# Kernel optimization log

Measured on AMD Instinct MI355X. Metric: run time of the kernel, lower is better.

## Reference

```python
import jax, jax.numpy as jnp
import numpy as np

N, E, F_IN, HD, H, G, NG, OUT = 50000, 800000, 128, 64, 4, 512, 50, 64
HC = HD * H  # 256
LN_EPS = 1e-5

def _lin(k, fi, fo):
    return jax.random.normal(k, (fi, fo), jnp.float32) / np.sqrt(fi).astype(np.float32)

def setup_inputs() -> dict:
    key = jax.random.key(0)
    ks = jax.random.split(key, 26)
    x = jax.random.normal(ks[0], (N, F_IN), jnp.float32)
    edge_index = jax.random.randint(ks[1], (2, E), 0, N)
    batch = jnp.sort(jax.random.randint(ks[2], (N,), 0, G))
    group_ids = jax.random.randint(ks[3], (N,), 0, NG)
    inp = {
        'x': x, 'edge_index': edge_index, 'batch': batch, 'group_ids': group_ids,
        'group_table': jax.random.normal(ks[4], (NG, HD), jnp.float32),
        'inW': _lin(ks[5], F_IN + HD, HD), 'inb': jnp.zeros((HD,), jnp.float32),
        'inln_g': jnp.ones((HD,), jnp.float32), 'inln_b': jnp.zeros((HD,), jnp.float32),
        'W0': _lin(ks[6], HD, HC), 'as0': jax.random.normal(ks[7], (H, HD), jnp.float32) * 0.1,
        'ad0': jax.random.normal(ks[8], (H, HD), jnp.float32) * 0.1, 'b0': jnp.zeros((HC,), jnp.float32),
        'ln0g': jnp.ones((HC,), jnp.float32), 'ln0b': jnp.zeros((HC,), jnp.float32),
        'W1': _lin(ks[9], HC, HC), 'as1': jax.random.normal(ks[10], (H, HD), jnp.float32) * 0.1,
        'ad1': jax.random.normal(ks[11], (H, HD), jnp.float32) * 0.1, 'b1': jnp.zeros((HC,), jnp.float32),
        'ln1g': jnp.ones((HC,), jnp.float32), 'ln1b': jnp.zeros((HC,), jnp.float32),
        'fc1W': _lin(ks[12], HC, HD), 'fc1b': jnp.zeros((HD,), jnp.float32),
        'fc2W': _lin(ks[13], HD, OUT), 'fc2b': jnp.zeros((OUT,), jnp.float32),
    }
    return inp

def _layer_norm(x, g, b):
    mu = jnp.mean(x, axis=-1, keepdims=True)
    var = jnp.mean(jnp.square(x - mu), axis=-1, keepdims=True)
    return (x - mu) * jax.lax.rsqrt(var + LN_EPS) * g + b

def _gat_conv(x, src, dst, W, a_src, a_dst, bias):
    # x: [N, Fin] -> per-head projection [N, H, HD]
    xl = (x @ W).reshape(-1, H, HD)
    al_s = jnp.einsum('nhc,hc->nh', xl, a_src)  # [N, H]
    al_d = jnp.einsum('nhc,hc->nh', xl, a_dst)
    e = jax.nn.leaky_relu(al_s[src] + al_d[dst], 0.2)  # [Etot, H]
    m = jax.ops.segment_max(e, dst, num_segments=N)    # stable softmax over in-edges
    ex = jnp.exp(e - m[dst])
    s = jax.ops.segment_sum(ex, dst, num_segments=N)
    alpha = ex / (s[dst] + 1e-16)
    msg = xl[src] * alpha[:, :, None]                   # [Etot, H, HD]
    out = jax.ops.segment_sum(msg, dst, num_segments=N)
    return out.reshape(-1, HC) + bias

def reference(x, edge_index, batch, group_ids, group_table, inW, inb, inln_g, inln_b,
              W0, as0, ad0, b0, ln0g, ln0b, W1, as1, ad1, b1, ln1g, ln1b,
              fc1W, fc1b, fc2W, fc2b):
    # group embedding concat + input projection (Linear -> LN -> GELU)
    h = jnp.concatenate([x, group_table[group_ids]], axis=-1)
    h = jax.nn.gelu(_layer_norm(h @ inW + inb, inln_g, inln_b), approximate=False)
    # add self-loops (PyG GATConv default)
    loop = jnp.arange(N)
    src = jnp.concatenate([edge_index[0], loop])
    dst = jnp.concatenate([edge_index[1], loop])
    # layer 0: dims 64 -> 256, no residual (width mismatch)
    h = jax.nn.gelu(_layer_norm(_gat_conv(h, src, dst, W0, as0, ad0, b0), ln0g, ln0b), approximate=False)
    # layer 1: 256 -> 256, residual applies
    identity = h
    h = jax.nn.gelu(_layer_norm(_gat_conv(h, src, dst, W1, as1, ad1, b1), ln1g, ln1b), approximate=False)
    h = h + identity
    # global mean pool over graphs
    sums = jax.ops.segment_sum(h, batch, num_segments=G)
    cnt = jax.ops.segment_sum(jnp.ones((N, 1), h.dtype), batch, num_segments=G)
    pooled = sums / jnp.maximum(cnt, 1.0)
    z = jax.nn.gelu(pooled @ fc1W + fc1b, approximate=False)
    logits = z @ fc2W + fc2b
    return jax.nn.log_softmax(logits, axis=1)
```

## Files before the change

kernel.cpp:

```cpp
#include <hip/hip_runtime.h>
#include <math.h>

#define N_NODES 50000
#define N_EDGES 800000
#define ETOT (N_EDGES + N_NODES)
#define F_IN 128
#define HD 64
#define NHEAD 4
#define HC 256
#define NGRAPH 512
#define NOUT 64
#define LN_EPS 1e-5f

typedef __attribute__((ext_vector_type(8))) short bf16x8;
typedef __attribute__((ext_vector_type(4))) float f32x4;
typedef __attribute__((ext_vector_type(2))) float f32x2;

__device__ __forceinline__ float wave_sum(float v) {
#pragma unroll
    for (int m = 1; m < 64; m <<= 1) v += __shfl_xor(v, m, 64);
    return v;
}
__device__ __forceinline__ float wave_max(float v) {
#pragma unroll
    for (int m = 1; m < 64; m <<= 1) v = fmaxf(v, __shfl_xor(v, m, 64));
    return v;
}
__device__ __forceinline__ float red16(float v) {
    v += __shfl_xor(v, 1, 64);
    v += __shfl_xor(v, 2, 64);
    v += __shfl_xor(v, 4, 64);
    v += __shfl_xor(v, 8, 64);
    return v;
}
__device__ __forceinline__ float gelu_exact(float x) {
    return 0.5f * x * (1.0f + erff(x * 0.70710678118654752f));
}
__device__ __forceinline__ unsigned short f2bf(float x) {
    unsigned int u = __float_as_uint(x);
    return (unsigned short)((u + 0x7fffu + ((u >> 16) & 1u)) >> 16);
}
__device__ __forceinline__ float bf2f(unsigned short u) {
    return __uint_as_float(((unsigned int)u) << 16);
}

__global__ void k_count(const int* __restrict__ ei, int* __restrict__ deg) {
    int t = blockIdx.x * blockDim.x + threadIdx.x;
    if (t >= ETOT) return;
    int dst = (t < N_EDGES) ? ei[N_EDGES + t] : (t - N_EDGES);
    atomicAdd(deg + dst, 1);
}

__global__ void k_scan(const int* __restrict__ deg, int* __restrict__ rowptr,
                       int* __restrict__ cursor) {
    __shared__ int wsum[16];
    __shared__ int chunk_total;
    int tid = threadIdx.x, wid = tid >> 6, lane = tid & 63;
    int carry = 0;
    if (tid == 0) rowptr[0] = 0;
    for (int base = 0; base < N_NODES; base += 1024) {
        int i = base + tid;
        int v = (i < N_NODES) ? deg[i] : 0;
        int incl = v;
#pragma unroll
        for (int off = 1; off < 64; off <<= 1) {
            int t = __shfl_up(incl, off, 64);
            if (lane >= off) incl += t;
        }
        if (lane == 63) wsum[wid] = incl;
        __syncthreads();
        if (wid == 0) {
            int wv = (lane < 16) ? wsum[lane] : 0;
            int wincl = wv;
#pragma unroll
            for (int off = 1; off < 16; off <<= 1) {
                int t = __shfl_up(wincl, off, 64);
                if (lane >= off) wincl += t;
            }
            if (lane < 16) wsum[lane] = wincl - wv;
            if (lane == 15) chunk_total = wincl;
        }
        __syncthreads();
        int total_incl = carry + wsum[wid] + incl;
        if (i < N_NODES) {
            rowptr[i + 1] = total_incl;
            cursor[i] = total_incl - v;
        }
        carry += chunk_total;
        __syncthreads();
    }
}

__global__ void k_fill(const int* __restrict__ ei, int* __restrict__ cursor,
                       int* __restrict__ csr) {
    int t = blockIdx.x * blockDim.x + threadIdx.x;
    if (t >= ETOT) return;
    int src, dst;
    if (t < N_EDGES) { src = ei[t]; dst = ei[N_EDGES + t]; }
    else             { src = t - N_EDGES; dst = src; }
    int p = atomicAdd(cursor + dst, 1);
    csr[p] = src;
}

__global__ void k_pack_all(const float* __restrict__ inW, const float* __restrict__ W0,
                           const float* __restrict__ W1, const float* __restrict__ as0,
                           const float* __restrict__ ad0,
                           unsigned short* __restrict__ inWpk, unsigned short* __restrict__ W0pk,
                           unsigned short* __restrict__ W1pk, float* __restrict__ us,
                           float* __restrict__ ud) {
    int b = blockIdx.x;
    if (b < 48) {
        int tid = b * 256 + threadIdx.x;
        int i = tid & 7, l = (tid >> 3) & 63, t2 = tid >> 9;
        int nb = t2 % 4, kt = t2 / 4;
        int k = kt * 32 + ((l >> 4) << 3) + i;
        int n = nb * 16 + (l & 15);
        inWpk[tid] = f2bf(inW[k * 64 + n]);
    } else if (b < 112) {
        int tid = (b - 48) * 256 + threadIdx.x;
        int i = tid & 7, l = (tid >> 3) & 63, t2 = tid >> 9;
        int nb = t2 % 16, kt = t2 / 16;
        int q = kt * 32 + ((l >> 4) << 3) + i;
        int k = 16 * (q & 3) + (q >> 2);
        int n = nb * 16 + (l & 15);
        W0pk[tid] = f2bf(W0[k * 256 + n]);
    } else if (b < 368) {
        int tid = (b - 112) * 256 + threadIdx.x;
        int i = tid & 7, l = (tid >> 3) & 63, t2 = tid >> 9;
        int nb = t2 % 16, kt = t2 / 16;
        int k = kt * 32 + ((l >> 4) << 3) + i;
        int n = nb * 16 + (l & 15);
        W1pk[tid] = f2bf(W1[k * 256 + n]);
    } else {
        int t = threadIdx.x;
        int h = t >> 6, k2 = t & 63;
        float ss = 0.f, dd = 0.f;
        for (int c = 0; c < 64; c++) {
            float w = W0[k2 * 256 + h * 64 + c];
            ss += w * as0[h * 64 + c];
            dd += w * ad0[h * 64 + c];
        }
        us[t] = ss;
        ud[t] = dd;
    }
}

__global__ void k_proj_in_mma(const float* __restrict__ x, const int* __restrict__ gid,
                              const float* __restrict__ gt,
                              const unsigned short* __restrict__ Wpk,
                              const float* __restrict__ inb, const float* __restrict__ lng,
                              const float* __restrict__ lnb, const float* __restrict__ us,
                              const float* __restrict__ ud, unsigned int* __restrict__ h08,
                              float* __restrict__ als0, float* __restrict__ ald0) {
    int wid = threadIdx.x >> 6, lane = threadIdx.x & 63;
    int m0 = blockIdx.x * 64 + wid * 16;
    if (m0 >= N_NODES) return;
    int g16 = lane >> 4, c16 = lane & 15;
    int row_a = m0 + c16;
    int g = gid[row_a];
    f32x4 acc[4] = {{0,0,0,0},{0,0,0,0},{0,0,0,0},{0,0,0,0}};
#pragma unroll
    for (int kt = 0; kt < 6; kt++) {
        const float* src = (kt < 4) ? (x + (size_t)row_a * F_IN + kt * 32 + g16 * 8)
                                    : (gt + (size_t)g * HD + (kt - 4) * 32 + g16 * 8);
        float4 f0 = *(const float4*)(src);
        float4 f1 = *(const float4*)(src + 4);
        bf16x8 a;
        a[0] = (short)f2bf(f0.x); a[1] = (short)f2bf(f0.y);
        a[2] = (short)f2bf(f0.z); a[3] = (short)f2bf(f0.w);
        a[4] = (short)f2bf(f1.x); a[5] = (short)f2bf(f1.y);
        a[6] = (short)f2bf(f1.z); a[7] = (short)f2bf(f1.w);
#pragma unroll
        for (int nt = 0; nt < 4; nt++) {
            bf16x8 b = *(const bf16x8*)(Wpk + (((kt * 4 + nt) * 64 + lane) << 3));
            acc[nt] = __builtin_amdgcn_mfma_f32_16x16x32_bf16(a, b, acc[nt], 0, 0, 0);
        }
    }
    float bv[4], gv[4], bb[4];
    float usl[4][4], udl[4][4];
#pragma unroll
    for (int nt = 0; nt < 4; nt++) {
        int c = nt * 16 + c16;
        bv[nt] = inb[c]; gv[nt] = lng[c]; bb[nt] = lnb[c];
#pragma unroll
        for (int h = 0; h < 4; h++) {
            usl[h][nt] = us[h * 64 + c];
            udl[h][nt] = ud[h * 64 + c];
        }
    }
#pragma unroll
    for (int j = 0; j < 4; j++) {
        float d[4], s = 0.f;
#pragma unroll
        for (int nt = 0; nt < 4; nt++) { d[nt] = acc[nt][j] + bv[nt]; s += d[nt]; }
        float mu = red16(s) * (1.0f / 64.0f);
        float v = 0.f;
#pragma unroll
        for (int nt = 0; nt < 4; nt++) { d[nt] -= mu; v += d[nt] * d[nt]; }
        float r = rsqrtf(red16(v) * (1.0f / 64.0f) + LN_EPS);
        int row = m0 + g16 * 4 + j;
        float y0 = gelu_exact(d[0] * r * gv[0] + bb[0]);
        float y1 = gelu_exact(d[1] * r * gv[1] + bb[1]);
        float y2 = gelu_exact(d[2] * r * gv[2] + bb[2]);
        float y3 = gelu_exact(d[3] * r * gv[3] + bb[3]);
        int u = __builtin_amdgcn_cvt_pk_fp8_f32(y0, y1, 0, false);
        u = __builtin_amdgcn_cvt_pk_fp8_f32(y2, y3, u, true);
        h08[(size_t)row * 16 + c16] = (unsigned int)u;
        float ps0 = y0 * usl[0][0] + y1 * usl[0][1] + y2 * usl[0][2] + y3 * usl[0][3];
        float ps1 = y0 * usl[1][0] + y1 * usl[1][1] + y2 * usl[1][2] + y3 * usl[1][3];
        float ps2 = y0 * usl[2][0] + y1 * usl[2][1] + y2 * usl[2][2] + y3 * usl[2][3];
        float ps3 = y0 * usl[3][0] + y1 * usl[3][1] + y2 * usl[3][2] + y3 * usl[3][3];
        float pd0 = y0 * udl[0][0] + y1 * udl[0][1] + y2 * udl[0][2] + y3 * udl[0][3];
        float pd1 = y0 * udl[1][0] + y1 * udl[1][1] + y2 * udl[1][2] + y3 * udl[1][3];
        float pd2 = y0 * udl[2][0] + y1 * udl[2][1] + y2 * udl[2][2] + y3 * udl[2][3];
        float pd3 = y0 * udl[3][0] + y1 * udl[3][1] + y2 * udl[3][2] + y3 * udl[3][3];
        ps0 = red16(ps0); ps1 = red16(ps1); ps2 = red16(ps2); ps3 = red16(ps3);
        pd0 = red16(pd0); pd1 = red16(pd1); pd2 = red16(pd2); pd3 = red16(pd3);
        if (c16 == 0) {
            float4 s4 = {ps0, ps1, ps2, ps3};
            float4 d4 = {pd0, pd1, pd2, pd3};
            ((float4*)als0)[row] = s4;
            ((float4*)ald0)[row] = d4;
        }
    }
}

__global__ void k_agg0(const int* __restrict__ rowptr, const int* __restrict__ csr,
                       const unsigned int* __restrict__ h08, const float* __restrict__ als,
                       const float* __restrict__ ald, unsigned short* __restrict__ aggbf) {
    __shared__ float4 lacc[2][64];
    __shared__ float lss[2][4];
    int wid = threadIdx.x >> 6, lane = threadIdx.x & 63;
    int nloc = wid >> 1, half = wid & 1;
    int node = blockIdx.x * 2 + nloc;
    int start = rowptr[node], end = rowptr[node + 1];
    int g = lane >> 4, l16 = lane & 15;
    float4 adv = ((const float4*)ald)[node];
    int cntE = end - start;
    int mid = start + ((cntE + 1) >> 1);
    int k0 = half ? mid : start;
    int k1 = half ? end : mid;
    float a00 = 0, a01 = 0, a02 = 0, a03 = 0;
    float a10 = 0, a11 = 0, a12 = 0, a13 = 0;
    float a20 = 0, a21 = 0, a22 = 0, a23 = 0;
    float a30 = 0, a31 = 0, a32 = 0, a33 = 0;
    float s0 = 0, s1 = 0, s2 = 0, s3 = 0;
    const float4* als4 = (const float4*)als;
    for (int kb = k0; kb < k1; kb += 8) {
        int eA = kb + g, eB = kb + 4 + g;
        int cA = (eA < k1) ? eA : (k1 - 1);
        int cB = (eB < k1) ? eB : (k1 - 1);
        int snA = csr[cA], snB = csr[cB];
        float4 avA = als4[snA], avB = als4[snB];
        unsigned int uA = h08[(size_t)snA * 16 + l16];
        unsigned int uB = h08[(size_t)snB * 16 + l16];
        float eA0 = avA.x + adv.x; eA0 = fmaxf(eA0, 0.2f * eA0);
        float eA1 = avA.y + adv.y; eA1 = fmaxf(eA1, 0.2f * eA1);
        float eA2 = avA.z + adv.z; eA2 = fmaxf(eA2, 0.2f * eA2);
        float eA3 = avA.w + adv.w; eA3 = fmaxf(eA3, 0.2f * eA3);
        float wA0 = __expf(eA0), wA1 = __expf(eA1), wA2 = __expf(eA2), wA3 = __expf(eA3);
        if (eA >= k1) { wA0 = 0.f; wA1 = 0.f; wA2 = 0.f; wA3 = 0.f; }
        f32x2 loA = __builtin_amdgcn_cvt_pk_f32_fp8((int)uA, false);
        f32x2 hiA = __builtin_amdgcn_cvt_pk_f32_fp8((int)uA, true);
        s0 += wA0; s1 += wA1; s2 += wA2; s3 += wA3;
        float x0 = loA.x, x1 = loA.y, x2 = hiA.x, x3 = hiA.y;
        a00 += wA0 * x0; a01 += wA0 * x1; a02 += wA0 * x2; a03 += wA0 * x3;
        a10 += wA1 * x0; a11 += wA1 * x1; a12 += wA1 * x2; a13 += wA1 * x3;
        a20 += wA2 * x0; a21 += wA2 * x1; a22 += wA2 * x2; a23 += wA2 * x3;
        a30 += wA3 * x0; a31 += wA3 * x1; a32 += wA3 * x2; a33 += wA3 * x3;
        float eB0 = avB.x + adv.x; eB0 = fmaxf(eB0, 0.2f * eB0);
        float eB1 = avB.y + adv.y; eB1 = fmaxf(eB1, 0.2f * eB1);
        float eB2 = avB.z + adv.z; eB2 = fmaxf(eB2, 0.2f * eB2);
        float eB3 = avB.w + adv.w; eB3 = fmaxf(eB3, 0.2f * eB3);
        float wB0 = __expf(eB0), wB1 = __expf(eB1), wB2 = __expf(eB2), wB3 = __expf(eB3);
        if (eB >= k1) { wB0 = 0.f; wB1 = 0.f; wB2 = 0.f; wB3 = 0.f; }
        f32x2 loB = __builtin_amdgcn_cvt_pk_f32_fp8((int)uB, false);
        f32x2 hiB = __builtin_amdgcn_cvt_pk_f32_fp8((int)uB, true);
        s0 += wB0; s1 += wB1; s2 += wB2; s3 += wB3;
        float z0 = loB.x, z1 = loB.y, z2 = hiB.x, z3 = hiB.y;
        a00 += wB0 * z0; a01 += wB0 * z1; a02 += wB0 * z2; a03 += wB0 * z3;
        a10 += wB1 * z0; a11 += wB1 * z1; a12 += wB1 * z2; a13 += wB1 * z3;
        a20 += wB2 * z0; a21 += wB2 * z1; a22 += wB2 * z2; a23 += wB2 * z3;
        a30 += wB3 * z0; a31 += wB3 * z1; a32 += wB3 * z2; a33 += wB3 * z3;
    }
#define RED2(v) v += __shfl_xor(v, 16, 64); v += __shfl_xor(v, 32, 64)
    RED2(a00); RED2(a01); RED2(a02); RED2(a03);
    RED2(a10); RED2(a11); RED2(a12); RED2(a13);
    RED2(a20); RED2(a21); RED2(a22); RED2(a23);
    RED2(a30); RED2(a31); RED2(a32); RED2(a33);
    RED2(s0);  RED2(s1);  RED2(s2);  RED2(s3);
#undef RED2
    if (half) {
        float o0 = (g == 0) ? a00 : (g == 1) ? a10 : (g == 2) ? a20 : a30;
        float o1 = (g == 0) ? a01 : (g == 1) ? a11 : (g == 2) ? a21 : a31;
        float o2 = (g == 0) ? a02 : (g == 1) ? a12 : (g == 2) ? a22 : a32;
        float o3 = (g == 0) ? a03 : (g == 1) ? a13 : (g == 2) ? a23 : a33;
        float4 o = {o0, o1, o2, o3};
        lacc[nloc][lane] = o;
        if (lane < 4) {
            float sv = (lane == 0) ? s0 : (lane == 1) ? s1 : (lane == 2) ? s2 : s3;
            lss[nloc][lane] = sv;
        }
    }
    __syncthreads();
    if (!half) {
        float4 p0 = lacc[nloc][0 + l16];
        float4 p1 = lacc[nloc][16 + l16];
        float4 p2 = lacc[nloc][32 + l16];
        float4 p3 = lacc[nloc][48 + l16];
        a00 += p0.x; a01 += p0.y; a02 += p0.z; a03 += p0.w;
        a10 += p1.x; a11 += p1.y; a12 += p1.z; a13 += p1.w;
        a20 += p2.x; a21 += p2.y; a22 += p2.z; a23 += p2.w;
        a30 += p3.x; a31 += p3.y; a32 += p3.z; a33 += p3.w;
        s0 += lss[nloc][0]; s1 += lss[nloc][1];
        s2 += lss[nloc][2]; s3 += lss[nloc][3];
        float o0 = (g == 0) ? a00 : (g == 1) ? a10 : (g == 2) ? a20 : a30;
        float o1 = (g == 0) ? a01 : (g == 1) ? a11 : (g == 2) ? a21 : a31;
        float o2 = (g == 0) ? a02 : (g == 1) ? a12 : (g == 2) ? a22 : a32;
        float o3 = (g == 0) ? a03 : (g == 1) ? a13 : (g == 2) ? a23 : a33;
        float sg = (g == 0) ? s0 : (g == 1) ? s1 : (g == 2) ? s2 : s3;
        float inv = 1.0f / (sg + 1e-16f);
        ushort4 o = {f2bf(o0 * inv), f2bf(o1 * inv), f2bf(o2 * inv), f2bf(o3 * inv)};
        ((ushort4*)aggbf)[(size_t)node * 64 + lane] = o;
    }
}

__global__ void k_postgemm0(const unsigned short* __restrict__ A,
                            const unsigned short* __restrict__ Wpk,
                            const float* __restrict__ bias, const float* __restrict__ lng,
                            const float* __restrict__ lnb, unsigned short* __restrict__ h1bf) {
    int wid = threadIdx.x >> 6, lane = threadIdx.x & 63;
    int m0 = blockIdx.x * 64 + wid * 16;
    if (m0 >= N_NODES) return;
    int g16 = lane >> 4, c16 = lane & 15;
    f32x4 acc[16] = {};
#pragma unroll
    for (int h = 0; h < 4; h++) {
#pragma unroll
        for (int kt = 0; kt < 2; kt++) {
            bf16x8 a = *(const bf16x8*)(A + (size_t)(m0 + c16) * 256 + h * 64 + kt * 32 + g16 * 8);
#pragma unroll
            for (int nt = 0; nt < 4; nt++) {
                bf16x8 b = *(const bf16x8*)(Wpk + (((kt * 16 + h * 4 + nt) * 64 + lane) << 3));
                acc[h * 4 + nt] = __builtin_amdgcn_mfma_f32_16x16x32_bf16(a, b, acc[h * 4 + nt], 0, 0, 0);
            }
        }
    }
    float bv[16], gv[16], bb[16];
#pragma unroll
    for (int q = 0; q < 16; q++) {
        int c = q * 16 + c16;
        bv[q] = bias[c]; gv[q] = lng[c]; bb[q] = lnb[c];
    }
#pragma unroll
    for (int j = 0; j < 4; j++) {
        float d[16], ssum = 0.f;
#pragma unroll
        for (int q = 0; q < 16; q++) { d[q] = acc[q][j] + bv[q]; ssum += d[q]; }
        float mu = red16(ssum) * (1.0f / 256.0f);
        float v = 0.f;
#pragma unroll
        for (int q = 0; q < 16; q++) { d[q] -= mu; v += d[q] * d[q]; }
        float r = rsqrtf(red16(v) * (1.0f / 256.0f) + LN_EPS);
        int row = m0 + g16 * 4 + j;
#pragma unroll
        for (int q = 0; q < 16; q++) {
            float y = gelu_exact(d[q] * r * gv[q] + bb[q]);
            h1bf[(size_t)row * 256 + q * 16 + c16] = f2bf(y);
        }
    }
}

__global__ void k_proj_mma(const unsigned short* __restrict__ A,
                           const unsigned short* __restrict__ Wpk,
                           const float* __restrict__ as_, const float* __restrict__ ad_,
                           unsigned int* __restrict__ xl8, float* __restrict__ als,
                           float* __restrict__ ald) {
    int wid = threadIdx.x >> 6, lane = threadIdx.x & 63;
    int m0 = blockIdx.x * 16;
    int g16 = lane >> 4, c16 = lane & 15;
    f32x4 acc[4] = {{0,0,0,0},{0,0,0,0},{0,0,0,0},{0,0,0,0}};
#pragma unroll
    for (int kt = 0; kt < 8; kt++) {
        bf16x8 a = *(const bf16x8*)(A + (size_t)(m0 + c16) * 256 + kt * 32 + g16 * 8);
#pragma unroll
        for (int nt = 0; nt < 4; nt++) {
            bf16x8 b = *(const bf16x8*)(Wpk + (((kt * 16 + wid * 4 + nt) * 64 + lane) << 3));
            acc[nt] = __builtin_amdgcn_mfma_f32_16x16x32_bf16(a, b, acc[nt], 0, 0, 0);
        }
    }
    float asv[4], adv[4];
#pragma unroll
    for (int nt = 0; nt < 4; nt++) {
        int c = wid * 64 + nt * 16 + c16;
        asv[nt] = as_[c]; adv[nt] = ad_[c];
    }
#pragma unroll
    for (int j = 0; j < 4; j++) {
        int row = m0 + g16 * 4 + j;
        float v0 = acc[0][j], v1 = acc[1][j], v2 = acc[2][j], v3 = acc[3][j];
        int u = __builtin_amdgcn_cvt_pk_fp8_f32(v0, v1, 0, false);
        u = __builtin_amdgcn_cvt_pk_fp8_f32(v2, v3, u, true);
        xl8[(size_t)row * 64 + wid * 16 + c16] = (unsigned int)u;
        float ps = v0 * asv[0] + v1 * asv[1] + v2 * asv[2] + v3 * asv[3];
        float pd = v0 * adv[0] + v1 * adv[1] + v2 * adv[2] + v3 * adv[3];
        ps = red16(ps); pd = red16(pd);
        if (c16 == 0) { als[row * 4 + wid] = ps; ald[row * 4 + wid] = pd; }
    }
}

__global__ void k_agg1(const int* __restrict__ rowptr, const int* __restrict__ csr,
                       const unsigned int* __restrict__ xl8, const float* __restrict__ als,
                       const float* __restrict__ ald, const float* __restrict__ bias,
                       const float* __restrict__ lng, const float* __restrict__ lnb,
                       const unsigned short* __restrict__ identity_bf,
                       const int* __restrict__ batch, float* __restrict__ pooled,
                       int* __restrict__ cnt) {
    __shared__ float4 lacc[2][3][64];
    __shared__ float lss[2][3][64];
    __shared__ float4 lyout[2][64];
    __shared__ int lbatch[2];
    int wid = threadIdx.x >> 6, lane = threadIdx.x & 63;
    int nloc = wid >> 2, q = wid & 3;
    int node = blockIdx.x * 2 + nloc;
    int start = rowptr[node], end = rowptr[node + 1];
    int len = end - start;
    int head = lane >> 4, c16 = lane & 15;
    int fb = head * 64 + c16;
    float adh = ald[node * 4 + head];
    int k0 = start + (len * q) / 4;
    int k1 = start + (len * (q + 1)) / 4;
    float4 acc = {0.f, 0.f, 0.f, 0.f};
    float s = 0.f;
    int k = k0;
    for (; k + 4 <= k1; k += 4) {
        int sn0 = csr[k], sn1 = csr[k + 1], sn2 = csr[k + 2], sn3 = csr[k + 3];
        float e0 = als[sn0 * 4 + head] + adh;
        float e1 = als[sn1 * 4 + head] + adh;
        float e2 = als[sn2 * 4 + head] + adh;
        float e3 = als[sn3 * 4 + head] + adh;
        unsigned int u0 = xl8[(size_t)sn0 * 64 + lane];
        unsigned int u1 = xl8[(size_t)sn1 * 64 + lane];
        unsigned int u2 = xl8[(size_t)sn2 * 64 + lane];
        unsigned int u3 = xl8[(size_t)sn3 * 64 + lane];
        e0 = fmaxf(e0, 0.2f * e0); e1 = fmaxf(e1, 0.2f * e1);
        e2 = fmaxf(e2, 0.2f * e2); e3 = fmaxf(e3, 0.2f * e3);
        float a0 = __expf(e0), a1 = __expf(e1), a2 = __expf(e2), a3 = __expf(e3);
        s += a0 + a1 + a2 + a3;
        f32x2 lo0 = __builtin_amdgcn_cvt_pk_f32_fp8((int)u0, false);
        f32x2 hi0 = __builtin_amdgcn_cvt_pk_f32_fp8((int)u0, true);
        f32x2 lo1 = __builtin_amdgcn_cvt_pk_f32_fp8((int)u1, false);
        f32x2 hi1 = __builtin_amdgcn_cvt_pk_f32_fp8((int)u1, true);
        f32x2 lo2 = __builtin_amdgcn_cvt_pk_f32_fp8((int)u2, false);
        f32x2 hi2 = __builtin_amdgcn_cvt_pk_f32_fp8((int)u2, true);
        f32x2 lo3 = __builtin_amdgcn_cvt_pk_f32_fp8((int)u3, false);
        f32x2 hi3 = __builtin_amdgcn_cvt_pk_f32_fp8((int)u3, true);
        acc.x += a0 * lo0.x + a1 * lo1.x + a2 * lo2.x + a3 * lo3.x;
        acc.y += a0 * lo0.y + a1 * lo1.y + a2 * lo2.y + a3 * lo3.y;
        acc.z += a0 * hi0.x + a1 * hi1.x + a2 * hi2.x + a3 * hi3.x;
        acc.w += a0 * hi0.y + a1 * hi1.y + a2 * hi2.y + a3 * hi3.y;
    }
    for (; k < k1; k++) {
        int sn = csr[k];
        float e = als[sn * 4 + head] + adh;
        e = fmaxf(e, 0.2f * e);
        float a = __expf(e);
        s += a;
        unsigned int u = xl8[(size_t)sn * 64 + lane];
        f32x2 lo = __builtin_amdgcn_cvt_pk_f32_fp8((int)u, false);
        f32x2 hi = __builtin_amdgcn_cvt_pk_f32_fp8((int)u, true);
        acc.x += a * lo.x; acc.y += a * lo.y;
        acc.z += a * hi.x; acc.w += a * hi.y;
    }
    if (q) { lacc[nloc][q - 1][lane] = acc; lss[nloc][q - 1][lane] = s; }
    __syncthreads();
    if (q == 0) {
        float4 p0 = lacc[nloc][0][lane];
        float4 p1 = lacc[nloc][1][lane];
        float4 p2 = lacc[nloc][2][lane];
        acc.x += p0.x + p1.x + p2.x;
        acc.y += p0.y + p1.y + p2.y;
        acc.z += p0.z + p1.z + p2.z;
        acc.w += p0.w + p1.w + p2.w;
        s += lss[nloc][0][lane] + lss[nloc][1][lane] + lss[nloc][2][lane];
        float inv = 1.0f / (s + 1e-16f);
        acc.x = acc.x * inv + bias[fb];
        acc.y = acc.y * inv + bias[fb + 16];
        acc.z = acc.z * inv + bias[fb + 32];
        acc.w = acc.w * inv + bias[fb + 48];
        float mu = wave_sum(acc.x + acc.y + acc.z + acc.w) * (1.0f / 256.0f);
        float dx = acc.x - mu, dy = acc.y - mu, dz = acc.z - mu, dw = acc.w - mu;
        float var = wave_sum(dx * dx + dy * dy + dz * dz + dw * dw) * (1.0f / 256.0f);
        float r = rsqrtf(var + LN_EPS);
        float g0v = lng[fb], g1v = lng[fb + 16], g2v = lng[fb + 32], g3v = lng[fb + 48];
        float b0v = lnb[fb], b1v = lnb[fb + 16], b2v = lnb[fb + 32], b3v = lnb[fb + 48];
        const unsigned short* idp = identity_bf + (size_t)node * 256 + fb;
        float4 y;
        y.x = gelu_exact(dx * r * g0v + b0v) + bf2f(idp[0]);
        y.y = gelu_exact(dy * r * g1v + b1v) + bf2f(idp[16]);
        y.z = gelu_exact(dz * r * g2v + b2v) + bf2f(idp[32]);
        y.w = gelu_exact(dw * r * g3v + b3v) + bf2f(idp[48]);
        lyout[nloc][lane] = y;
        if (lane == 0) lbatch[nloc] = batch[node];
    }
    __syncthreads();
    if (wid == 0) {
        int g0 = lbatch[0], g1 = lbatch[1];
        float4 a = lyout[0][lane], b = lyout[1][lane];
        float* p0 = pooled + (size_t)g0 * 256 + fb;
        if (g0 == g1) {
            atomicAdd(p0 +  0, a.x + b.x); atomicAdd(p0 + 16, a.y + b.y);
            atomicAdd(p0 + 32, a.z + b.z); atomicAdd(p0 + 48, a.w + b.w);
            if (lane == 0) atomicAdd(cnt + g0, 2);
        } else {
            float* p1 = pooled + (size_t)g1 * 256 + fb;
            atomicAdd(p0 +  0, a.x); atomicAdd(p0 + 16, a.y);
            atomicAdd(p0 + 32, a.z); atomicAdd(p0 + 48, a.w);
            atomicAdd(p1 +  0, b.x); atomicAdd(p1 + 16, b.y);
            atomicAdd(p1 + 32, b.z); atomicAdd(p1 + 48, b.w);
            if (lane == 0) { atomicAdd(cnt + g0, 1); atomicAdd(cnt + g1, 1); }
        }
    }
}

__global__ void k_final(const float* __restrict__ pooled, const int* __restrict__ cnt,
                        const float* __restrict__ fc1W, const float* __restrict__ fc1b,
                        const float* __restrict__ fc2W, const float* __restrict__ fc2b,
                        float* __restrict__ out) {
    __shared__ float prow[4][256];
    __shared__ float zrow[4][64];
    int wid = threadIdx.x >> 6, lane = threadIdx.x & 63;
    int g = blockIdx.x * 4 + wid;
    float inv = 1.0f / fmaxf((float)cnt[g], 1.0f);
#pragma unroll
    for (int k = lane; k < 256; k += 64) prow[wid][k] = pooled[g * 256 + k] * inv;
    __syncthreads();
    float acc = fc1b[lane];
#pragma unroll 4
    for (int k = 0; k < 256; k++) acc += prow[wid][k] * fc1W[k * 64 + lane];
    zrow[wid][lane] = gelu_exact(acc);
    __syncthreads();
    float logit = fc2b[lane];
#pragma unroll 4
    for (int k = 0; k < 64; k++) logit += zrow[wid][k] * fc2W[k * 64 + lane];
    float mx = wave_max(logit);
    float se = wave_sum(__expf(logit - mx));
    out[g * NOUT + lane] = logit - mx - logf(se);
}

extern "C" void kernel_launch(void* const* d_in, const int* in_sizes, int n_in,
                              void* d_out, int out_size, void* d_ws, size_t ws_size,
                              hipStream_t stream) {
    const float* x     = (const float*)d_in[0];
    const int*   ei    = (const int*)d_in[1];
    const int*   batch = (const int*)d_in[2];
    const int*   gid   = (const int*)d_in[3];
    const float* gt    = (const float*)d_in[4];
    const float* inW   = (const float*)d_in[5];
    const float* inb   = (const float*)d_in[6];
    const float* inlng = (const float*)d_in[7];
    const float* inlnb = (const float*)d_in[8];
    const float* W0    = (const float*)d_in[9];
    const float* as0   = (const float*)d_in[10];
    const float* ad0   = (const float*)d_in[11];
    const float* b0    = (const float*)d_in[12];
    const float* ln0g  = (const float*)d_in[13];
    const float* ln0b  = (const float*)d_in[14];
    const float* W1    = (const float*)d_in[15];
    const float* as1   = (const float*)d_in[16];
    const float* ad1   = (const float*)d_in[17];
    const float* b1    = (const float*)d_in[18];
    const float* ln1g  = (const float*)d_in[19];
    const float* ln1b  = (const float*)d_in[20];
    const float* fc1W  = (const float*)d_in[21];
    const float* fc1b  = (const float*)d_in[22];
    const float* fc2W  = (const float*)d_in[23];
    const float* fc2b  = (const float*)d_in[24];
    float* out = (float*)d_out;

    char* ws = (char*)d_ws;
    size_t off = 0;
    auto alloc = [&](size_t bytes) {
        void* p = ws + off;
        off += (bytes + 255) / 256 * 256;
        return p;
    };
    unsigned int*   h08    = (unsigned int*)alloc((size_t)N_NODES * 16 * 4);
    unsigned short* agg0bf = (unsigned short*)alloc((size_t)N_NODES * 256 * 2);
    unsigned short* h1bf   = (unsigned short*)alloc((size_t)N_NODES * 256 * 2);
    unsigned int*   xl8    = (unsigned int*)alloc((size_t)N_NODES * 64 * 4);
    unsigned short* inWpk  = (unsigned short*)alloc((size_t)192 * 64 * 2);
    unsigned short* W0pk   = (unsigned short*)alloc((size_t)64 * 256 * 2);
    unsigned short* W1pk   = (unsigned short*)alloc((size_t)256 * 256 * 2);
    float* us     = (float*)alloc((size_t)256 * 4);
    float* ud     = (float*)alloc((size_t)256 * 4);
    float* als0   = (float*)alloc((size_t)N_NODES * 4 * 4);
    float* ald0   = (float*)alloc((size_t)N_NODES * 4 * 4);
    float* als1   = (float*)alloc((size_t)N_NODES * 4 * 4);
    float* ald1   = (float*)alloc((size_t)N_NODES * 4 * 4);
    int*   rowptr = (int*)alloc((size_t)(N_NODES + 1) * 4);
    int*   cursor = (int*)alloc((size_t)N_NODES * 4);
    int*   csr    = (int*)alloc((size_t)ETOT * 4);
    float* pooled = (float*)alloc((size_t)NGRAPH * 256 * 4);
    int*   cnt    = (int*)alloc((size_t)NGRAPH * 4);
    int*   deg    = (int*)alloc((size_t)N_NODES * 4);
    size_t zspan = ((char*)deg + (size_t)N_NODES * 4) - (char*)pooled;

    hipMemsetAsync(pooled, 0, zspan, stream);

    int eb = (ETOT + 255) / 256;
    k_count<<<eb, 256, 0, stream>>>(ei, deg);
    k_scan<<<1, 1024, 0, stream>>>(deg, rowptr, cursor);
    k_fill<<<eb, 256, 0, stream>>>(ei, cursor, csr);

    k_pack_all<<<369, 256, 0, stream>>>(inW, W0, W1, as0, ad0, inWpk, W0pk, W1pk, us, ud);

    k_proj_in_mma<<<(N_NODES + 63) / 64, 256, 0, stream>>>(x, gid, gt, inWpk, inb, inlng, inlnb,
                                                           us, ud, h08, als0, ald0);
    k_agg0<<<N_NODES / 2, 256, 0, stream>>>(rowptr, csr, h08, als0, ald0, agg0bf);
    k_postgemm0<<<(N_NODES + 63) / 64, 256, 0, stream>>>(agg0bf, W0pk, b0, ln0g, ln0b, h1bf);
    k_proj_mma<<<N_NODES / 16, 256, 0, stream>>>(h1bf, W1pk, as1, ad1, xl8, als1, ald1);
    k_agg1<<<N_NODES / 2, 512, 0, stream>>>(rowptr, csr, xl8, als1, ald1, b1, ln1g, ln1b,
                                            h1bf, batch, pooled, cnt);
    k_final<<<NGRAPH / 4, 256, 0, stream>>>(pooled, cnt, fc1W, fc1b, fc2W, fc2b, out);
}
```

Before: 435.6 us.

## Split layer-1 aggregation into per-head gather kernel and separate LN/pool kernel

Replaces the fused layer-1 aggregation with two kernels. The first gives each head its own block, splits edges between two waves, and has each 16-lane group take one edge so four edges are gathered at once. It writes normalized per-head sums as bf16 to a new buffer. The second kernel applies bias, LayerNorm, GELU and the residual, then pools with atomics, merging four nodes into one atomic when they share a graph. This aims to raise gather parallelism and cut per-block reduction overhead, at the cost of an extra global round trip and a kernel launch.

```diff
diff --git a/kernel.cpp b/kernel.cpp
--- a/kernel.cpp
+++ b/kernel.cpp
@@ -409,117 +409,120 @@
     }
 }
 
-__global__ void k_agg1(const int* __restrict__ rowptr, const int* __restrict__ csr,
-                       const unsigned int* __restrict__ xl8, const float* __restrict__ als,
-                       const float* __restrict__ ald, const float* __restrict__ bias,
-                       const float* __restrict__ lng, const float* __restrict__ lnb,
-                       const unsigned short* __restrict__ identity_bf,
-                       const int* __restrict__ batch, float* __restrict__ pooled,
-                       int* __restrict__ cnt) {
-    __shared__ float4 lacc[2][3][64];
-    __shared__ float lss[2][3][64];
-    __shared__ float4 lyout[2][64];
-    __shared__ int lbatch[2];
+__global__ void k_agg1g(const int* __restrict__ rowptr, const int* __restrict__ csr,
+                        const unsigned int* __restrict__ xl8, const float* __restrict__ als,
+                        const float* __restrict__ ald, unsigned short* __restrict__ partial) {
+    __shared__ float4 lacc[2][16];
+    __shared__ float lssm[2][16];
+    int bid = blockIdx.x;
+    int h = bid & 3;
+    int pair = bid >> 2;
     int wid = threadIdx.x >> 6, lane = threadIdx.x & 63;
-    int nloc = wid >> 2, q = wid & 3;
-    int node = blockIdx.x * 2 + nloc;
+    int nloc = wid >> 1, half = wid & 1;
+    int node = pair * 2 + nloc;
     int start = rowptr[node], end = rowptr[node + 1];
-    int len = end - start;
+    int g = lane >> 4, l16 = lane & 15;
+    float adh = ald[node * 4 + h];
+    int cntE = end - start;
+    int mid = start + ((cntE + 1) >> 1);
+    int k0 = half ? mid : start;
+    int k1 = half ? end : mid;
+    float a0 = 0, a1 = 0, a2 = 0, a3 = 0, s = 0;
+    for (int kb = k0; kb < k1; kb += 8) {
+        int eA = kb + g, eB = kb + 4 + g;
+        int cA = (eA < k1) ? eA : (k1 - 1);
+        int cB = (eB < k1) ? eB : (k1 - 1);
+        int snA = csr[cA], snB = csr[cB];
+        float evA = als[snA * 4 + h] + adh;
+        float evB = als[snB * 4 + h] + adh;
+        unsigned int uA = xl8[(size_t)snA * 64 + h * 16 + l16];
+        unsigned int uB = xl8[(size_t)snB * 64 + h * 16 + l16];
+        evA = fmaxf(evA, 0.2f * evA);
+        evB = fmaxf(evB, 0.2f * evB);
+        float wA = __expf(evA), wB = __expf(evB);
+        if (eA >= k1) wA = 0.f;
+        if (eB >= k1) wB = 0.f;
+        f32x2 loA = __builtin_amdgcn_cvt_pk_f32_fp8((int)uA, false);
+        f32x2 hiA = __builtin_amdgcn_cvt_pk_f32_fp8((int)uA, true);
+        f32x2 loB = __builtin_amdgcn_cvt_pk_f32_fp8((int)uB, false);
+        f32x2 hiB = __builtin_amdgcn_cvt_pk_f32_fp8((int)uB, true);
+        s += wA + wB;
+        a0 += wA * loA.x + wB * loB.x;
+        a1 += wA * loA.y + wB * loB.y;
+        a2 += wA * hiA.x + wB * hiB.x;
+        a3 += wA * hiA.y + wB * hiB.y;
+    }
+    a0 += __shfl_xor(a0, 16, 64); a0 += __shfl_xor(a0, 32, 64);
+    a1 += __shfl_xor(a1, 16, 64); a1 += __shfl_xor(a1, 32, 64);
+    a2 += __shfl_xor(a2, 16, 64); a2 += __shfl_xor(a2, 32, 64);
+    a3 += __shfl_xor(a3, 16, 64); a3 += __shfl_xor(a3, 32, 64);
+    s  += __shfl_xor(s, 16, 64);  s  += __shfl_xor(s, 32, 64);
+    if (half && g == 0) {
+        float4 o = {a0, a1, a2, a3};
+        lacc[nloc][l16] = o;
+        lssm[nloc][l16] = s;
+    }
+    __syncthreads();
+    if (!half && g == 0) {
+        float4 p = lacc[nloc][l16];
+        a0 += p.x; a1 += p.y; a2 += p.z; a3 += p.w;
+        s += lssm[nloc][l16];
+        float inv = 1.0f / (s + 1e-16f);
+        ushort4 o = {f2bf(a0 * inv), f2bf(a1 * inv), f2bf(a2 * inv), f2bf(a3 * inv)};
+        ((ushort4*)partial)[(size_t)node * 64 + h * 16 + l16] = o;
+    }
+}
+
+__global__ void k_ln1(const unsigned short* __restrict__ partial, const float* __restrict__ bias,
+                      const float* __restrict__ lng, const float* __restrict__ lnb,
+                      const unsigned short* __restrict__ identity_bf,
+                      const int* __restrict__ batch, float* __restrict__ pooled,
+                      int* __restrict__ cnt) {
+    __shared__ float4 ly[4][64];
+    __shared__ int lb[4];
+    int wid = threadIdx.x >> 6, lane = threadIdx.x & 63;
+    int node = blockIdx.x * 4 + wid;
     int head = lane >> 4, c16 = lane & 15;
     int fb = head * 64 + c16;
-    float adh = ald[node * 4 + head];
-    int k0 = start + (len * q) / 4;
-    int k1 = start + (len * (q + 1)) / 4;
-    float4 acc = {0.f, 0.f, 0.f, 0.f};
-    float s = 0.f;
-    int k = k0;
-    for (; k + 4 <= k1; k += 4) {
-        int sn0 = csr[k], sn1 = csr[k + 1], sn2 = csr[k + 2], sn3 = csr[k + 3];
-        float e0 = als[sn0 * 4 + head] + adh;
-        float e1 = als[sn1 * 4 + head] + adh;
-        float e2 = als[sn2 * 4 + head] + adh;
-        float e3 = als[sn3 * 4 + head] + adh;
-        unsigned int u0 = xl8[(size_t)sn0 * 64 + lane];
-        unsigned int u1 = xl8[(size_t)sn1 * 64 + lane];
-        unsigned int u2 = xl8[(size_t)sn2 * 64 + lane];
-        unsigned int u3 = xl8[(size_t)sn3 * 64 + lane];
-        e0 = fmaxf(e0, 0.2f * e0); e1 = fmaxf(e1, 0.2f * e1);
-        e2 = fmaxf(e2, 0.2f * e2); e3 = fmaxf(e3, 0.2f * e3);
-        float a0 = __expf(e0), a1 = __expf(e1), a2 = __expf(e2), a3 = __expf(e3);
-        s += a0 + a1 + a2 + a3;
-        f32x2 lo0 = __builtin_amdgcn_cvt_pk_f32_fp8((int)u0, false);
-        f32x2 hi0 = __builtin_amdgcn_cvt_pk_f32_fp8((int)u0, true);
-        f32x2 lo1 = __builtin_amdgcn_cvt_pk_f32_fp8((int)u1, false);
-        f32x2 hi1 = __builtin_amdgcn_cvt_pk_f32_fp8((int)u1, true);
-        f32x2 lo2 = __builtin_amdgcn_cvt_pk_f32_fp8((int)u2, false);
-        f32x2 hi2 = __builtin_amdgcn_cvt_pk_f32_fp8((int)u2, true);
-        f32x2 lo3 = __builtin_amdgcn_cvt_pk_f32_fp8((int)u3, false);
-        f32x2 hi3 = __builtin_amdgcn_cvt_pk_f32_fp8((int)u3, true);
-        acc.x += a0 * lo0.x + a1 * lo1.x + a2 * lo2.x + a3 * lo3.x;
-        acc.y += a0 * lo0.y + a1 * lo1.y + a2 * lo2.y + a3 * lo3.y;
-        acc.z += a0 * hi0.x + a1 * hi1.x + a2 * hi2.x + a3 * hi3.x;
-        acc.w += a0 * hi0.y + a1 * hi1.y + a2 * hi2.y + a3 * hi3.y;
-    }
-    for (; k < k1; k++) {
-        int sn = csr[k];
-        float e = als[sn * 4 + head] + adh;
-        e = fmaxf(e, 0.2f * e);
-        float a = __expf(e);
-        s += a;
-        unsigned int u = xl8[(size_t)sn * 64 + lane];
-        f32x2 lo = __builtin_amdgcn_cvt_pk_f32_fp8((int)u, false);
-        f32x2 hi = __builtin_amdgcn_cvt_pk_f32_fp8((int)u, true);
-        acc.x += a * lo.x; acc.y += a * lo.y;
-        acc.z += a * hi.x; acc.w += a * hi.y;
-    }
-    if (q) { lacc[nloc][q - 1][lane] = acc; lss[nloc][q - 1][lane] = s; }
+    ushort4 pv = ((const ushort4*)partial)[(size_t)node * 64 + lane];
+    float ax = bf2f(pv.x) + bias[fb];
+    float ay = bf2f(pv.y) + bias[fb + 16];
+    float az = bf2f(pv.z) + bias[fb + 32];
+    float aw = bf2f(pv.w) + bias[fb + 48];
+    float mu = wave_sum(ax + ay + az + aw) * (1.0f / 256.0f);
+    float dx = ax - mu, dy = ay - mu, dz = az - mu, dw = aw - mu;
+    float var = wave_sum(dx * dx + dy * dy + dz * dz + dw * dw) * (1.0f / 256.0f);
+    float r = rsqrtf(var + LN_EPS);
+    float g0v = lng[fb], g1v = lng[fb + 16], g2v = lng[fb + 32], g3v = lng[fb + 48];
+    float b0v = lnb[fb], b1v = lnb[fb + 16], b2v = lnb[fb + 32], b3v = lnb[fb + 48];
+    const unsigned short* idp = identity_bf + (size_t)node * 256 + fb;
+    float4 y;
+    y.x = gelu_exact(dx * r * g0v + b0v) + bf2f(idp[0]);
+    y.y = gelu_exact(dy * r * g1v + b1v) + bf2f(idp[16]);
+    y.z = gelu_exact(dz * r * g2v + b2v) + bf2f(idp[32]);
+    y.w = gelu_exact(dw * r * g3v + b3v) + bf2f(idp[48]);
+    int b = batch[node];
+    ly[wid][lane] = y;
+    if (lane == 0) lb[wid] = b;
     __syncthreads();
-    if (q == 0) {
-        float4 p0 = lacc[nloc][0][lane];
-        float4 p1 = lacc[nloc][1][lane];
-        float4 p2 = lacc[nloc][2][lane];
-        acc.x += p0.x + p1.x + p2.x;
-        acc.y += p0.y + p1.y + p2.y;
-        acc.z += p0.z + p1.z + p2.z;
-        acc.w += p0.w + p1.w + p2.w;
-        s += lss[nloc][0][lane] + lss[nloc][1][lane] + lss[nloc][2][lane];
-        float inv = 1.0f / (s + 1e-16f);
-        acc.x = acc.x * inv + bias[fb];
-        acc.y = acc.y * inv + bias[fb + 16];
-        acc.z = acc.z * inv + bias[fb + 32];
-        acc.w = acc.w * inv + bias[fb + 48];
-        float mu = wave_sum(acc.x + acc.y + acc.z + acc.w) * (1.0f / 256.0f);
-        float dx = acc.x - mu, dy = acc.y - mu, dz = acc.z - mu, dw = acc.w - mu;
-        float var = wave_sum(dx * dx + dy * dy + dz * dz + dw * dw) * (1.0f / 256.0f);
-        float r = rsqrtf(var + LN_EPS);
-        float g0v = lng[fb], g1v = lng[fb + 16], g2v = lng[fb + 32], g3v = lng[fb + 48];
-        float b0v = lnb[fb], b1v = lnb[fb + 16], b2v = lnb[fb + 32], b3v = lnb[fb + 48];
-        const unsigned short* idp = identity_bf + (size_t)node * 256 + fb;
-        float4 y;
-        y.x = gelu_exact(dx * r * g0v + b0v) + bf2f(idp[0]);
-        y.y = gelu_exact(dy * r * g1v + b1v) + bf2f(idp[16]);
-        y.z = gelu_exact(dz * r * g2v + b2v) + bf2f(idp[32]);
-        y.w = gelu_exact(dw * r * g3v + b3v) + bf2f(idp[48]);
-        lyout[nloc][lane] = y;
-        if (lane == 0) lbatch[nloc] = batch[node];
-    }
-    __syncthreads();
-    if (wid == 0) {
-        int g0 = lbatch[0], g1 = lbatch[1];
-        float4 a = lyout[0][lane], b = lyout[1][lane];
-        float* p0 = pooled + (size_t)g0 * 256 + fb;
-        if (g0 == g1) {
-            atomicAdd(p0 +  0, a.x + b.x); atomicAdd(p0 + 16, a.y + b.y);
-            atomicAdd(p0 + 32, a.z + b.z); atomicAdd(p0 + 48, a.w + b.w);
-            if (lane == 0) atomicAdd(cnt + g0, 2);
-        } else {
-            float* p1 = pooled + (size_t)g1 * 256 + fb;
-            atomicAdd(p0 +  0, a.x); atomicAdd(p0 + 16, a.y);
-            atomicAdd(p0 + 32, a.z); atomicAdd(p0 + 48, a.w);
-            atomicAdd(p1 +  0, b.x); atomicAdd(p1 + 16, b.y);
-            atomicAdd(p1 + 32, b.z); atomicAdd(p1 + 48, b.w);
-            if (lane == 0) { atomicAdd(cnt + g0, 1); atomicAdd(cnt + g1, 1); }
-        }
+    bool merged = (lb[0] == lb[1]) && (lb[1] == lb[2]) && (lb[2] == lb[3]);
+    if (merged) {
+        if (wid == 0) {
+            float4 y0 = ly[0][lane], y1 = ly[1][lane], y2 = ly[2][lane], y3 = ly[3][lane];
+            float* p = pooled + (size_t)lb[0] * 256 + fb;
+            atomicAdd(p +  0, y0.x + y1.x + y2.x + y3.x);
+            atomicAdd(p + 16, y0.y + y1.y + y2.y + y3.y);
+            atomicAdd(p + 32, y0.z + y1.z + y2.z + y3.z);
+            atomicAdd(p + 48, y0.w + y1.w + y2.w + y3.w);
+            if (lane == 0) atomicAdd(cnt + lb[0], 4);
+        }
+    } else {
+        float* p = pooled + (size_t)b * 256 + fb;
+        atomicAdd(p +  0, y.x);
+        atomicAdd(p + 16, y.y);
+        atomicAdd(p + 32, y.z);
+        atomicAdd(p + 48, y.w);
+        if (lane == 0) atomicAdd(cnt + b, 1);
     }
 }
 
@@ -589,6 +592,7 @@
     unsigned short* agg0bf = (unsigned short*)alloc((size_t)N_NODES * 256 * 2);
     unsigned short* h1bf   = (unsigned short*)alloc((size_t)N_NODES * 256 * 2);
     unsigned int*   xl8    = (unsigned int*)alloc((size_t)N_NODES * 64 * 4);
+    unsigned short* part1  = (unsigned short*)alloc((size_t)N_NODES * 256 * 2);
     unsigned short* inWpk  = (unsigned short*)alloc((size_t)192 * 64 * 2);
     unsigned short* W0pk   = (unsigned short*)alloc((size_t)64 * 256 * 2);
     unsigned short* W1pk   = (unsigned short*)alloc((size_t)256 * 256 * 2);
@@ -620,7 +624,7 @@
     k_agg0<<<N_NODES / 2, 256, 0, stream>>>(rowptr, csr, h08, als0, ald0, agg0bf);
     k_postgemm0<<<(N_NODES + 63) / 64, 256, 0, stream>>>(agg0bf, W0pk, b0, ln0g, ln0b, h1bf);
     k_proj_mma<<<N_NODES / 16, 256, 0, stream>>>(h1bf, W1pk, as1, ad1, xl8, als1, ald1);
-    k_agg1<<<N_NODES / 2, 512, 0, stream>>>(rowptr, csr, xl8, als1, ald1, b1, ln1g, ln1b,
-                                            h1bf, batch, pooled, cnt);
+    k_agg1g<<<(N_NODES / 2) * 4, 256, 0, stream>>>(rowptr, csr, xl8, als1, ald1, part1);
+    k_ln1<<<N_NODES / 4, 256, 0, stream>>>(part1, b1, ln1g, ln1b, h1bf, batch, pooled, cnt);
     k_final<<<NGRAPH / 4, 256, 0, stream>>>(pooled, cnt, fc1W, fc1b, fc2W, fc2b, out);
 }
```

Result: slower. 454.1 us (+4.3%).
